# Kernel tuning notes

Measured on AMD Instinct MI355X. Metric: run time of the kernel, lower is better.

The kernel has to match this reference:

```python
import jax, jax.numpy as jnp
from jax import lax
import numpy as np


def _conv(x, w, stride):
    # x: [B,C,D,H,W], w: [3,3,3,Cin,Cout]; kernel 3, pad 1 (matches SubMConv3d / SparseConv3d(3, s, padding=1))
    return lax.conv_general_dilated(x, w, (stride, stride, stride), [(1, 1)] * 3,
                                    dimension_numbers=('NCDHW', 'DHWIO', 'NCDHW'))


def _bn_relu(y, scale, shift, mask):
    # eval-mode BatchNorm folded to scale/shift, ReLU, then restrict to active sites
    return jnp.maximum(y * scale[None, :, None, None, None] + shift[None, :, None, None, None], 0.0) * mask


def _downsample_mask(m):
    # SparseConv3d(k=3, s=2, p=1): output site active iff any input in its 3x3x3 window is active
    return lax.reduce_window(m, -jnp.inf, lax.max, (1, 1, 3, 3, 3), (1, 1, 2, 2, 2),
                             [(0, 0), (0, 0), (1, 1), (1, 1), (1, 1)])


def setup_inputs() -> dict:
    key = jax.random.key(0)
    ks = jax.random.split(key, 40)
    B, D = 1, 128
    occ = jax.random.uniform(ks[0], (B, 1, D, D, D)) < 0.05
    x = jax.random.normal(ks[1], (B, 16, D, D, D), jnp.float32) * occ

    def w(k, ci, co):
        return jax.random.normal(k, (3, 3, 3, ci, co), jnp.float32) * (1.0 / np.sqrt(27.0 * ci))

    def sc(k, c):
        return jax.random.uniform(k, (c,), jnp.float32, 0.5, 1.5)

    def sh(k, c):
        return jax.random.normal(k, (c,), jnp.float32) * 0.1

    chans = [(16, 16), (16, 16), (16, 32), (32, 32), (32, 32), (32, 64), (64, 64), (64, 64), (64, 64)]
    names = ['w0a', 'w0b', 'wd0', 'w1a', 'w1b', 'wd1', 'w2a', 'w2b', 'w2c']
    d = {'x': x, 'mask': occ}
    i = 2
    for n, (ci, co) in zip(names, chans):
        d[n] = w(ks[i], ci, co)
        d['s' + n[1:]] = sc(ks[i + 1], co)
        d['b' + n[1:]] = sh(ks[i + 2], co)
        i += 3
    return d


def reference(x, mask, w0a, s0a, b0a, w0b, s0b, b0b, wd0, sd0, bd0,
              w1a, s1a, b1a, w1b, s1b, b1b, wd1, sd1, bd1,
              w2a, s2a, b2a, w2b, s2b, b2b, w2c, s2c, b2c):
    m0 = mask.astype(x.dtype)                       # active sites at full res [B,1,128,128,128]
    h = _bn_relu(_conv(x, w0a, 1), s0a, b0a, m0)    # conv0 (subm0)
    h = _bn_relu(_conv(h, w0b, 1), s0b, b0b, m0)
    m1 = _downsample_mask(m0)                       # down0 activity [B,1,64,64,64]
    h = _bn_relu(_conv(h, wd0, 2), sd0, bd0, m1)
    h = _bn_relu(_conv(h, w1a, 1), s1a, b1a, m1)    # conv1 (subm1)
    h = _bn_relu(_conv(h, w1b, 1), s1b, b1b, m1)
    m2 = _downsample_mask(m1)                       # down1 activity [B,1,32,32,32]
    h = _bn_relu(_conv(h, wd1, 2), sd1, bd1, m2)
    h = _bn_relu(_conv(h, w2a, 1), s2a, b2a, m2)    # conv2 (subm2)
    h = _bn_relu(_conv(h, w2b, 1), s2b, b2b, m2)
    h = _bn_relu(_conv(h, w2c, 1), s2c, b2c, m2)
    return h                                        # .dense() -> [B,64,32,32,32]
```

## Files before the change

kernel.cpp:

```cpp
#include <hip/hip_runtime.h>
#include <cstdint>

typedef unsigned short u16;
typedef unsigned int u32;
typedef unsigned char u8;
typedef unsigned long long u64;
typedef __attribute__((ext_vector_type(8))) short short8;
typedef __attribute__((ext_vector_type(4))) float f32x4;

#define CAP 131072

__device__ __forceinline__ float bf1(u16 v){ union{u32 i; float f;} c; c.i = ((u32)v) << 16; return c.f; }
__device__ __forceinline__ u16 f2bf(float f){
    union{float f; u32 i;} c; c.f = f; u32 i = c.i;
    return (u16)((i + 0x7FFFu + ((i >> 16) & 1u)) >> 16);
}

constexpr int ilog2c(int n){ return n <= 1 ? 0 : 1 + ilog2c(n / 2); }

struct PAll {
    const void* w[9];
    u32 wstart[10];
    int cin[9], cout[9], mode[9];
    const void* s[18];
};

__global__ void detect_k(const u16* __restrict__ s0a, u32* __restrict__ flag){
    if (threadIdx.x == 0){
        int ok = 1;
        #pragma unroll
        for (int i = 0; i < 8; i += 2){
            u16 v = s0a[i];
            if (v < 0x3F00u || v > 0x3FC0u) ok = 0;
        }
        flag[0] = ok ? 1u : 0u;
    }
}

__global__ __launch_bounds__(256)
void prep_k(PAll J, u16* __restrict__ FR, float* __restrict__ S,
            const u32* __restrict__ flag){
    const int gi = blockIdx.x * 256 + threadIdx.x;
    const int wtot = (int)J.wstart[9];
    if (gi < wtot){
        int j = 0;
        while (gi >= (int)J.wstart[j + 1]) ++j;
        const int i = gi - (int)J.wstart[j];
        const void* w = J.w[j];
        const int CIN = J.cin[j], COUT = J.cout[j];
        const int jj = i & 7;
        const int lane = (i >> 3) & 63;
        int rest = i >> 9;
        int src = -1;
        if (J.mode[j] == 0){
            const int KC = CIN >> 5, NT = COUT >> 4;
            const int nt = rest % NT; rest /= NT;
            const int kc = rest % KC; const int tap = rest / KC;
            const int k = kc * 32 + (lane >> 4) * 8 + jj;
            const int co = nt * 16 + (lane & 15);
            src = (tap * CIN + k) * COUT + co;
        } else if (J.mode[j] == 1){
            const int nt = rest & 1; const int pair = rest >> 1;
            const int kg = (lane >> 4) * 8 + jj;
            const int tap = pair * 2 + (kg >> 4);
            const int ci = kg & 15;
            const int co = nt * 16 + (lane & 15);
            if (tap < 27) src = (tap * 16 + ci) * 32 + co;
        } else {
            const int pair = rest;
            const int kg = (lane >> 4) * 8 + jj;
            const int tap = pair * 2 + (kg >> 4);
            const int ci = kg & 15;
            const int co = lane & 15;
            if (tap < 27) src = (tap * 16 + ci) * 16 + co;
        }
        float v = 0.f;
        if (src >= 0) v = flag[0] ? bf1(((const u16*)w)[src]) : ((const float*)w)[src];
        FR[gi] = f2bf(v);
    } else {
        const int i2 = gi - wtot;
        const int len[18] = {16,16,16,16,32,32,32,32,32,32,64,64,64,64,64,64,64,64};
        const int off[18] = {0,16,32,48,64,96,128,160,192,224,256,320,384,448,512,576,640,704};
        if (i2 < 768){
            int b = 0, base = 0;
            while (i2 >= base + len[b]) { base += len[b]; ++b; }
            const int t = i2 - base;
            const float v = flag[0] ? bf1(((const u16*)J.s[b])[t]) : ((const float*)J.s[b])[t];
            S[off[b] + t] = v;
        }
    }
}

__global__ __launch_bounds__(256)
void actmask_k(const void* __restrict__ xv, u64* __restrict__ bmask,
               u32* __restrict__ bcnt, const u32* __restrict__ flag){
    const int v = blockIdx.x * 256 + threadIdx.x;
    const size_t N = 2097152;
    u32 a = 0;
    if (flag[0]) {
        const u16* x = (const u16*)xv;
        #pragma unroll
        for (int c = 0; c < 16; ++c) a |= (u32)(x[(size_t)c * N + v]) & 0x7FFFu;
    } else {
        const u32* x = (const u32*)xv;
        #pragma unroll
        for (int c = 0; c < 16; ++c) a |= x[(size_t)c * N + v] & 0x7FFFFFFFu;
    }
    const u64 m = __ballot(a != 0);
    __shared__ u32 wc[4];
    const int lane = threadIdx.x & 63, wv = threadIdx.x >> 6;
    if (lane == 0) { bmask[v >> 6] = m; wc[wv] = (u32)__popcll(m); }
    __syncthreads();
    if (threadIdx.x == 0) bcnt[blockIdx.x] = wc[0] + wc[1] + wc[2] + wc[3];
}

__global__ __launch_bounds__(1024)
void aux_k(const u32* __restrict__ bcnt, u32* __restrict__ boff, u32* __restrict__ cnt,
           const u64* __restrict__ bmask, u8* __restrict__ m1){
    if (blockIdx.x == 0){
        __shared__ u32 lds[1024];
        const int t = threadIdx.x;
        u32 loc[8]; u32 s = 0;
        #pragma unroll
        for (int i = 0; i < 8; ++i){ loc[i] = s; s += bcnt[t * 8 + i]; }
        lds[t] = s;
        __syncthreads();
        u32 v = s;
        for (int d = 1; d < 1024; d <<= 1){
            u32 o = (t >= d) ? lds[t - d] : 0;
            __syncthreads();
            v += o; lds[t] = v;
            __syncthreads();
        }
        const u32 base = v - s;
        #pragma unroll
        for (int i = 0; i < 8; ++i) boff[t * 8 + i] = base + loc[i];
        if (t == 1023) cnt[0] = v;
    } else {
        const int v = (blockIdx.x - 1) * 1024 + threadIdx.x;
        const int xo = v & 63, yo = (v >> 6) & 63, zo = v >> 12;
        u32 a = 0;
        #pragma unroll
        for (int kz = 0; kz < 3; ++kz){ const int iz = 2*zo + kz - 1; if ((unsigned)iz >= 128u) continue;
          #pragma unroll
          for (int ky = 0; ky < 3; ++ky){ const int iy = 2*yo + ky - 1; if ((unsigned)iy >= 128u) continue;
            #pragma unroll
            for (int kx = 0; kx < 3; ++kx){ const int ix = 2*xo + kx - 1; if ((unsigned)ix >= 128u) continue;
              const int vv = (iz * 128 + iy) * 128 + ix;
              a |= (u32)((bmask[vv >> 6] >> (vv & 63)) & 1ull);
        }}}
        m1[v] = (u8)a;
    }
}

__global__ __launch_bounds__(256)
void scatter2m_k(const void* __restrict__ xv, const u64* __restrict__ bmask,
                 const u32* __restrict__ boff, int* __restrict__ idxmap,
                 int* __restrict__ alist, u16* __restrict__ f,
                 const u32* __restrict__ flag,
                 const u8* __restrict__ m1, u8* __restrict__ m2){
    if (blockIdx.x < 8192){
        const int v = blockIdx.x * 256 + threadIdx.x;
        const int lane = threadIdx.x & 63, wv = threadIdx.x >> 6;
        const u64 m = bmask[v >> 6];
        __shared__ u32 wc[4];
        if (lane == 0) wc[wv] = (u32)__popcll(m);
        __syncthreads();
        u32 wbase = 0;
        for (int i = 0; i < wv; ++i) wbase += wc[i];
        const bool act = (m >> lane) & 1ull;
        const u32 rank = (u32)__popcll(m & ((1ull << lane) - 1ull));
        int slot = -1;
        if (act){
            const u32 sl = boff[blockIdx.x] + wbase + rank;
            if (sl < CAP){
                slot = (int)sl;
                alist[slot] = v;
                if (flag[0]){
                    const u16* x = (const u16*)xv;
                    #pragma unroll
                    for (int c = 0; c < 16; ++c) f[(size_t)slot * 16 + c] = x[(size_t)c * 2097152 + v];
                } else {
                    const float* x = (const float*)xv;
                    #pragma unroll
                    for (int c = 0; c < 16; ++c) f[(size_t)slot * 16 + c] = f2bf(x[(size_t)c * 2097152 + v]);
                }
            }
        }
        idxmap[v] = slot;
    } else {
        const int v = (int)(blockIdx.x - 8192) * 256 + threadIdx.x;
        const int xo = v & 31, yo = (v >> 5) & 31, zo = v >> 10;
        u8 a = 0;
        #pragma unroll
        for (int kz = 0; kz < 3; ++kz){ const int iz = 2*zo + kz - 1; if ((unsigned)iz >= 64u) continue;
          #pragma unroll
          for (int ky = 0; ky < 3; ++ky){ const int iy = 2*yo + ky - 1; if ((unsigned)iy >= 64u) continue;
            #pragma unroll
            for (int kx = 0; kx < 3; ++kx){ const int ix = 2*xo + kx - 1; if ((unsigned)ix >= 64u) continue;
              a |= m1[((size_t)iz * 64 + iy) * 64 + ix];
        }}}
        m2[v] = a;
    }
}

__global__ __launch_bounds__(256)
void sconvm_k(const u16* __restrict__ fin, const int* __restrict__ idxmap,
              const int* __restrict__ alist, const u32* __restrict__ cnt,
              const u16* __restrict__ wf, const float* __restrict__ sc,
              const float* __restrict__ sh, u16* __restrict__ fout){
    const int n = min((int)cnt[0], CAP);
    const int j = blockIdx.x * 4 + (threadIdx.x >> 6);
    const int sbase = j * 16;
    if (sbase >= n) return;
    const int lane = threadIdx.x & 63;
    const int m = lane & 15, quad = lane >> 4;

    const int s = sbase + m;
    const int v = (s < n) ? alist[s] : -1;
    int xo = 0, yo = 0, zo = 0;
    if (v >= 0){ xo = v & 127; yo = (v >> 7) & 127; zo = v >> 14; }

    f32x4 acc = {0.f,0.f,0.f,0.f};
    #pragma unroll
    for (int p = 0; p < 14; ++p){
        const int tp = p * 2 + (quad >> 1);
        short8 a = {0,0,0,0,0,0,0,0};
        if (v >= 0 && tp < 27){
            const int kz = tp / 9, ky = (tp / 3) % 3, kx = tp % 3;
            const int iz = zo + kz - 1, iy = yo + ky - 1, ix = xo + kx - 1;
            if ((unsigned)iz < 128u && (unsigned)iy < 128u && (unsigned)ix < 128u){
                const int sn = idxmap[((size_t)iz * 128 + iy) * 128 + ix];
                if (sn >= 0) a = *(const short8*)(fin + (size_t)sn * 16 + (quad & 1) * 8);
            }
        }
        short8 b = *(const short8*)(wf + ((size_t)p * 64 + lane) * 8);
        acc = __builtin_amdgcn_mfma_f32_16x16x32_bf16(a, b, acc, 0, 0, 0);
    }

    const int co = lane & 15;
    const float scl = sc[co], shf = sh[co];
    #pragma unroll
    for (int r = 0; r < 4; ++r){
        const int srow = sbase + quad * 4 + r;
        if (srow < n){
            fout[(size_t)srow * 16 + co] = f2bf(fmaxf(acc[r] * scl + shf, 0.f));
        }
    }
}

__global__ __launch_bounds__(256)
void convd0m_k(const u16* __restrict__ fbuf, const int* __restrict__ idxmap,
               const u16* __restrict__ wf, const float* __restrict__ sc,
               const float* __restrict__ sh, const u8* __restrict__ mk,
               u16* __restrict__ out)
{
    const int wj = blockIdx.x * 4 + (threadIdx.x >> 6);
    const int lane = threadIdx.x & 63;
    const int m = lane & 15, quad = lane >> 4;
    const int xo_b = (wj & 3) * 16;
    const int yo = (wj >> 2) & 63;
    const int zo = wj >> 8;

    f32x4 acc0 = {0.f,0.f,0.f,0.f}, acc1 = {0.f,0.f,0.f,0.f};
    const int ix_m = (xo_b + m) * 2 - 1;

    #pragma unroll
    for (int p = 0; p < 14; ++p){
        const int tp = p * 2 + (quad >> 1);
        short8 a = {0,0,0,0,0,0,0,0};
        if (tp < 27){
            const int kz = tp / 9, ky = (tp / 3) % 3, kx = tp % 3;
            const int iz = 2*zo + kz - 1, iy = 2*yo + ky - 1, ix = ix_m + kx;
            if ((unsigned)iz < 128u && (unsigned)iy < 128u && (unsigned)ix < 128u){
                const int sn = idxmap[((size_t)iz * 128 + iy) * 128 + ix];
                if (sn >= 0) a = *(const short8*)(fbuf + (size_t)sn * 16 + (quad & 1) * 8);
            }
        }
        short8 b0 = *(const short8*)(wf + ((size_t)(p*2+0) * 64 + lane) * 8);
        short8 b1 = *(const short8*)(wf + ((size_t)(p*2+1) * 64 + lane) * 8);
        acc0 = __builtin_amdgcn_mfma_f32_16x16x32_bf16(a, b0, acc0, 0, 0, 0);
        acc1 = __builtin_amdgcn_mfma_f32_16x16x32_bf16(a, b1, acc1, 0, 0, 0);
    }

    const int vb = wj * 16 + quad * 4;
    const u32 m4 = *(const u32*)(mk + vb);
    const int n = lane & 15;
    #pragma unroll
    for (int nt = 0; nt < 2; ++nt){
        const int co = nt * 16 + n;
        const float s = sc[co], h = sh[co];
        const f32x4 acc = nt ? acc1 : acc0;
        #pragma unroll
        for (int r = 0; r < 4; ++r){
            float val = fmaxf(acc[r] * s + h, 0.f);
            val = ((m4 >> (8*r)) & 0xFFu) ? val : 0.f;
            out[(size_t)(vb + r) * 32 + co] = f2bf(val);
        }
    }
}

template<int DIN, int DOUT, int CIN, int COUT, int STRIDE, bool FINAL>
__global__ __launch_bounds__(256)
void mconv_k(const u16* __restrict__ in, const u16* __restrict__ wf,
             const float* __restrict__ sc, const float* __restrict__ sh,
             const u8* __restrict__ mk, void* __restrict__ out,
             const u32* __restrict__ flag)
{
    constexpr int KC = CIN / 32;
    constexpr int NT = COUT / 16;
    constexpr int XT = DOUT / 16;
    const int wj = blockIdx.x * 4 + (threadIdx.x >> 6);
    const int lane = threadIdx.x & 63;
    const int m = lane & 15, quad = lane >> 4;

    const int xo_b = (wj % XT) * 16;
    const int yo = (wj / XT) % DOUT;
    const int zo = wj / (XT * DOUT);

    f32x4 acc[NT];
    #pragma unroll
    for (int i = 0; i < NT; ++i) acc[i] = (f32x4){0.f,0.f,0.f,0.f};

    const int ix0 = (xo_b + m) * STRIDE - 1;
    for (int kz = 0; kz < 3; ++kz){
      const int iz = zo * STRIDE + kz - 1;
      if ((unsigned)iz >= (unsigned)DIN) continue;
      for (int ky = 0; ky < 3; ++ky){
        const int iy = yo * STRIDE + ky - 1;
        if ((unsigned)iy >= (unsigned)DIN) continue;
        const size_t rowb = ((size_t)iz * DIN + iy) * DIN;
        #pragma unroll
        for (int kx = 0; kx < 3; ++kx){
          const int ix = ix0 + kx;
          const bool v = (unsigned)ix < (unsigned)DIN;
          const int tap = (kz*3 + ky)*3 + kx;
          const u16* ap = in + (rowb + ix) * CIN + quad * 8;
          const u16* bp = wf + (size_t)tap * KC * NT * 512 + lane * 8;
          #pragma unroll
          for (int kc = 0; kc < KC; ++kc){
            short8 a = {0,0,0,0,0,0,0,0};
            if (v) a = *(const short8*)(ap + kc * 32);
            #pragma unroll
            for (int nt = 0; nt < NT; ++nt){
              short8 b = *(const short8*)(bp + (kc * NT + nt) * 512);
              acc[nt] = __builtin_amdgcn_mfma_f32_16x16x32_bf16(a, b, acc[nt], 0, 0, 0);
            }
          }
    }}}

    const int vb = wj * 16 + quad * 4;
    const u32 m4 = *(const u32*)(mk + vb);
    const int n = lane & 15;
    #pragma unroll
    for (int nt = 0; nt < NT; ++nt){
        const int co = nt * 16 + n;
        const float s = sc[co], h = sh[co];
        #pragma unroll
        for (int r = 0; r < 4; ++r){
            float val = fmaxf(acc[nt][r] * s + h, 0.f);
            val = ((m4 >> (8*r)) & 0xFFu) ? val : 0.f;
            ((u16*)out)[(size_t)(vb + r) * COUT + co] = f2bf(val);
        }
    }
    (void)flag;
}

template<int D, int CIN, int COUT, int WAVES, bool FINAL>
__global__ __launch_bounds__(WAVES*64)
void mconvlds_k(const u16* __restrict__ in, const u16* __restrict__ wf,
                const float* __restrict__ sc, const float* __restrict__ sh,
                const u8* __restrict__ mk, void* __restrict__ out,
                const u32* __restrict__ flag)
{
    constexpr int KC = CIN / 32;
    constexpr int NT = COUT / 16;
    constexpr int CH8 = CIN / 8;
    constexpr int BT = WAVES * 64;
    __shared__ u16 tile[9 * 2048];

    const int t = threadIdx.x;
    const int yo = blockIdx.x % D, zo = blockIdx.x / D;

    for (int dz = 0; dz < 3; ++dz){
      const int iz = zo + dz - 1;
      for (int dy = 0; dy < 3; ++dy){
        const int iy = yo + dy - 1;
        if ((unsigned)iz < (unsigned)D && (unsigned)iy < (unsigned)D){
          const u16* src = in + ((size_t)(iz * D + iy) * D) * CIN;
          u16* dst = &tile[(dz * 3 + dy) * 2048];
          for (int c = t; c < D * CH8; c += BT){
            const int x = c / CH8, c8 = c % CH8;
            *(short8*)(dst + (c8 * D + x) * 8) = *(const short8*)(src + c * 8);
          }
        }
      }
    }
    __syncthreads();

    const int lane = t & 63, w = t >> 6;
    const int m = lane & 15, quad = lane >> 4;
    const int xo_b = w * 16;

    f32x4 acc[NT];
    #pragma unroll
    for (int i = 0; i < NT; ++i) acc[i] = (f32x4){0.f,0.f,0.f,0.f};

    #pragma unroll
    for (int kz = 0; kz < 3; ++kz){
      const int iz = zo + kz - 1;
      if ((unsigned)iz >= (unsigned)D) continue;
      #pragma unroll
      for (int ky = 0; ky < 3; ++ky){
        const int iy = yo + ky - 1;
        if ((unsigned)iy >= (unsigned)D) continue;
        const u16* row = &tile[(kz * 3 + ky) * 2048];
        #pragma unroll
        for (int kx = 0; kx < 3; ++kx){
          const int ix = xo_b + m + kx - 1;
          const bool aok = (unsigned)ix < (unsigned)D;
          const int tap = (kz * 3 + ky) * 3 + kx;
          const u16* bp = wf + (size_t)tap * KC * NT * 512 + lane * 8;
          #pragma unroll
          for (int kc = 0; kc < KC; ++kc){
            short8 a = {0,0,0,0,0,0,0,0};
            if (aok) a = *(const short8*)(row + ((kc * 4 + quad) * D + ix) * 8);
            #pragma unroll
            for (int nt = 0; nt < NT; ++nt){
              short8 b = *(const short8*)(bp + (kc * NT + nt) * 512);
              acc[nt] = __builtin_amdgcn_mfma_f32_16x16x32_bf16(a, b, acc[nt], 0, 0, 0);
            }
          }
        }
      }
    }

    const int vb = (zo * D + yo) * D + xo_b + quad * 4;
    const u32 m4 = *(const u32*)(mk + vb);
    const int n = lane & 15;
    if (FINAL) {
        const bool bfout = flag[0] != 0;
        #pragma unroll
        for (int nt = 0; nt < NT; ++nt){
            const int co = nt * 16 + n;
            const float s = sc[co], h = sh[co];
            float4 o;
            float* po = &o.x;
            #pragma unroll
            for (int r = 0; r < 4; ++r){
                float val = fmaxf(acc[nt][r] * s + h, 0.f);
                po[r] = ((m4 >> (8*r)) & 0xFFu) ? val : 0.f;
            }
            if (!bfout) {
                *(float4*)((float*)out + (size_t)co * (D*D*D) + vb) = o;
            } else {
                u16* ob = (u16*)out + (size_t)co * (D*D*D) + vb;
                #pragma unroll
                for (int r = 0; r < 4; ++r) ob[r] = f2bf(po[r]);
            }
        }
    } else {
        #pragma unroll
        for (int nt = 0; nt < NT; ++nt){
            const int co = nt * 16 + n;
            const float s = sc[co], h = sh[co];
            #pragma unroll
            for (int r = 0; r < 4; ++r){
                float val = fmaxf(acc[nt][r] * s + h, 0.f);
                val = ((m4 >> (8*r)) & 0xFFu) ? val : 0.f;
                ((u16*)out)[(size_t)(vb + r) * COUT + co] = f2bf(val);
            }
        }
    }
}

extern "C" void kernel_launch(void* const* d_in, const int* in_sizes, int n_in,
                              void* d_out, int out_size, void* d_ws, size_t ws_size,
                              hipStream_t stream)
{
    (void)out_size; (void)ws_size;

    int wb = 2;
    for (int i = 1; i < n_in; ++i) { if (in_sizes[i] == 6912) { wb = i; break; } }

    const void* x = d_in[0];
    const void *w0a=d_in[wb+0],  *s0a=d_in[wb+1],  *b0a=d_in[wb+2];
    const void *w0b=d_in[wb+3],  *s0b=d_in[wb+4],  *b0b=d_in[wb+5];
    const void *wd0=d_in[wb+6],  *sd0=d_in[wb+7],  *bd0=d_in[wb+8];
    const void *w1a=d_in[wb+9],  *s1a=d_in[wb+10], *b1a=d_in[wb+11];
    const void *w1b=d_in[wb+12], *s1b=d_in[wb+13], *b1b=d_in[wb+14];
    const void *wd1=d_in[wb+15], *sd1=d_in[wb+16], *bd1=d_in[wb+17];
    const void *w2a=d_in[wb+18], *s2a=d_in[wb+19], *b2a=d_in[wb+20];
    const void *w2b=d_in[wb+21], *s2b=d_in[wb+22], *b2b=d_in[wb+23];
    const void *w2c=d_in[wb+24], *s2c=d_in[wb+25], *b2c=d_in[wb+26];

    char* ws = (char*)d_ws;
    int*   idxmap = (int*)(ws);
    u16*   Fb0    = (u16*)(ws + 8388608);
    u16*   Fb1    = (u16*)(ws + 12582912);
    u16*   Fb2    = (u16*)(ws + 16777216);
    u16*   Rb1    = (u16*)(ws + 25165824);
    u16*   Rb2    = (u16*)(ws + 41943040);
    u8*    m1     = (u8*)(ws + 58720256);
    u8*    m2     = (u8*)(ws + 58982400);
    u32*   cnt    = (u32*)(ws + 59015168);
    int*   alist  = (int*)(ws + 59015424);
    u16*   FR     = (u16*)(ws + 59539712);
    float* S      = (float*)(ws + 60483328);
    u32*   flag   = (u32*)(ws + 60486400);
    u64*   bmask  = (u64*)(ws + 60486656);
    u32*   bcnt   = (u32*)(ws + 60748800);
    u32*   boff   = (u32*)(ws + 60781568);

    u16* wfs0a = FR + 0;
    u16* wfs0b = FR + 7168;
    u16* fd0   = FR + 14336;
    u16* f1a   = FR + 28672;
    u16* f1b   = FR + 56320;
    u16* fd1   = FR + 83968;
    u16* f2a   = FR + 139264;
    u16* f2b   = FR + 249856;
    u16* f2c   = FR + 360448;

    detect_k<<<1, 64, 0, stream>>>((const u16*)s0a, flag);

    PAll J;
    const void* jsrc[9] = {w0a, w0b, wd0, w1a, w1b, wd1, w2a, w2b, w2c};
    const u32 jlen[9]   = {7168,7168,14336,27648,27648,55296,110592,110592,110592};
    const int jcin[9]   = {16,16,16,32,32,32,64,64,64};
    const int jcout[9]  = {16,16,32,32,32,64,64,64,64};
    const int jmode[9]  = {2,2,1,0,0,0,0,0,0};
    u32 acc = 0;
    for (int i = 0; i < 9; ++i){
        J.w[i] = jsrc[i]; J.wstart[i] = acc; acc += jlen[i];
        J.cin[i] = jcin[i]; J.cout[i] = jcout[i]; J.mode[i] = jmode[i];
    }
    J.wstart[9] = acc;
    const void* sv[18] = {s0a,b0a,s0b,b0b,sd0,bd0,s1a,b1a,s1b,b1b,sd1,bd1,s2a,b2a,s2b,b2b,s2c,b2c};
    for (int i = 0; i < 18; ++i) J.s[i] = sv[i];
    const u32 ptot = acc + 768;
    prep_k<<<(int)((ptot + 255) / 256), 256, 0, stream>>>(J, FR, S, flag);

    float *cs0a=S+0,  *cb0a=S+16,  *cs0b=S+32,  *cb0b=S+48;
    float *csd0=S+64, *cbd0=S+96,  *cs1a=S+128, *cb1a=S+160, *cs1b=S+192, *cb1b=S+224;
    float *csd1=S+256,*cbd1=S+320, *cs2a=S+384, *cb2a=S+448, *cs2b=S+512, *cb2b=S+576, *cs2c=S+640, *cb2c=S+704;

    actmask_k<<<8192, 256, 0, stream>>>(x, bmask, bcnt, flag);
    aux_k<<<257, 1024, 0, stream>>>(bcnt, boff, cnt, bmask, m1);
    scatter2m_k<<<8320, 256, 0, stream>>>(x, bmask, boff, idxmap, alist, Fb0, flag, m1, m2);

    sconvm_k<<<2048, 256, 0, stream>>>(Fb0, idxmap, alist, cnt, wfs0a, cs0a, cb0a, Fb1);
    sconvm_k<<<2048, 256, 0, stream>>>(Fb1, idxmap, alist, cnt, wfs0b, cs0b, cb0b, Fb2);
    convd0m_k<<<4096, 256, 0, stream>>>(Fb2, idxmap, fd0, csd0, cbd0, m1, Rb1);
    mconvlds_k<64,32,32,4,false><<<4096, 256, 0, stream>>>(Rb1, f1a, cs1a, cb1a, m1, Rb2, flag);
    mconvlds_k<64,32,32,4,false><<<4096, 256, 0, stream>>>(Rb2, f1b, cs1b, cb1b, m1, Rb1, flag);
    mconv_k<64,32,32,64,2,false><<<512, 256, 0, stream>>>(Rb1, fd1, csd1, cbd1, m2, Rb2, flag);
    mconvlds_k<32,64,64,2,false><<<1024, 128, 0, stream>>>(Rb2, f2a, cs2a, cb2a, m2, Rb1, flag);
    mconvlds_k<32,64,64,2,false><<<1024, 128, 0, stream>>>(Rb1, f2b, cs2b, cb2b, m2, Rb2, flag);
    mconvlds_k<32,64,64,2,true ><<<1024, 128, 0, stream>>>(Rb2, f2c, cs2c, cb2c, m2, d_out, flag);
}
```

Before: 530.9 us.

## Use 32x32x16 MFMA dense conv kernel for subm1 and subm2 layers

Adds a new dense convolution kernel that stages a 3x3 row neighbourhood in LDS and computes with 32x32x16 bf16 MFMA instructions, plus a new weight fragment layout (mode 3) matching that instruction. It replaces the previous 16-wide MFMA LDS kernel for four of the stride-1 layers. The aim is to raise MFMA throughput per instruction and cut fragment loads. B fragments are read directly from global memory each step, and the block size changes to 128 threads, which may alter occupancy and reuse.

```diff
diff --git a/kernel.cpp b/kernel.cpp
--- a/kernel.cpp
+++ b/kernel.cpp
@@ -7,6 +7,7 @@
 typedef unsigned long long u64;
 typedef __attribute__((ext_vector_type(8))) short short8;
 typedef __attribute__((ext_vector_type(4))) float f32x4;
+typedef __attribute__((ext_vector_type(16))) float f32x16;
 
 #define CAP 131072
 
@@ -66,13 +67,20 @@
             const int ci = kg & 15;
             const int co = nt * 16 + (lane & 15);
             if (tap < 27) src = (tap * 16 + ci) * 32 + co;
-        } else {
+        } else if (J.mode[j] == 2){
             const int pair = rest;
             const int kg = (lane >> 4) * 8 + jj;
             const int tap = pair * 2 + (kg >> 4);
             const int ci = kg & 15;
             const int co = lane & 15;
             if (tap < 27) src = (tap * 16 + ci) * 16 + co;
+        } else {
+            const int KC = CIN >> 4, NTN = COUT >> 5;
+            const int nt = rest % NTN; rest /= NTN;
+            const int kc = rest % KC; const int tap = rest / KC;
+            const int k = kc * 16 + (lane >> 5) * 8 + jj;
+            const int co = nt * 32 + (lane & 31);
+            src = (tap * CIN + k) * COUT + co;
         }
         float v = 0.f;
         if (src >= 0) v = flag[0] ? bf1(((const u16*)w)[src]) : ((const float*)w)[src];
@@ -474,6 +482,85 @@
     }
 }
 
+template<int D, int CIN, int COUT>
+__global__ __launch_bounds__(128)
+void mconv32_k(const u16* __restrict__ in, const u16* __restrict__ wf,
+               const float* __restrict__ sc, const float* __restrict__ sh,
+               const u8* __restrict__ mk, u16* __restrict__ out)
+{
+    constexpr int KC = CIN / 16;
+    constexpr int NTN = COUT / 32;
+    constexpr int XW = D / 32;
+    constexpr int CH8 = CIN / 8;
+    __shared__ u16 tile[9 * 2048];
+
+    const int t = threadIdx.x;
+    const int yo = blockIdx.x % D, zo = blockIdx.x / D;
+
+    for (int dz = 0; dz < 3; ++dz){
+      const int iz = zo + dz - 1;
+      for (int dy = 0; dy < 3; ++dy){
+        const int iy = yo + dy - 1;
+        if ((unsigned)iz < (unsigned)D && (unsigned)iy < (unsigned)D){
+          const u16* src = in + ((size_t)(iz * D + iy) * D) * CIN;
+          u16* dst = &tile[(dz * 3 + dy) * 2048];
+          for (int c = t; c < D * CH8; c += 128){
+            const int x = c / CH8, c8 = c % CH8;
+            *(short8*)(dst + (c8 * D + x) * 8) = *(const short8*)(src + c * 8);
+          }
+        }
+      }
+    }
+    __syncthreads();
+
+    const int lane = t & 63, w = t >> 6;
+    const int m32 = lane & 31, half = lane >> 5;
+    const int xo_b = (XW == 2) ? w * 32 : 0;
+    const int nt   = (XW == 2) ? 0 : w;
+
+    f32x16 acc;
+    #pragma unroll
+    for (int i = 0; i < 16; ++i) acc[i] = 0.f;
+
+    #pragma unroll
+    for (int kz = 0; kz < 3; ++kz){
+      const int iz = zo + kz - 1;
+      if ((unsigned)iz >= (unsigned)D) continue;
+      #pragma unroll
+      for (int ky = 0; ky < 3; ++ky){
+        const int iy = yo + ky - 1;
+        if ((unsigned)iy >= (unsigned)D) continue;
+        const u16* row = &tile[(kz * 3 + ky) * 2048];
+        #pragma unroll
+        for (int kx = 0; kx < 3; ++kx){
+          const int ix = xo_b + m32 + kx - 1;
+          const bool aok = (unsigned)ix < (unsigned)D;
+          const int tap = (kz * 3 + ky) * 3 + kx;
+          const u16* bp = wf + ((size_t)tap * KC * NTN + nt) * 512 + lane * 8;
+          #pragma unroll
+          for (int kc = 0; kc < KC; ++kc){
+            short8 a = {0,0,0,0,0,0,0,0};
+            if (aok) a = *(const short8*)(row + ((kc * 2 + half) * D + ix) * 8);
+            short8 b = *(const short8*)(bp + (size_t)kc * NTN * 512);
+            acc = __builtin_amdgcn_mfma_f32_32x32x16_bf16(a, b, acc, 0, 0, 0);
+          }
+        }
+      }
+    }
+
+    const int base = (zo * D + yo) * D;
+    const int co = nt * 32 + m32;
+    const float s = sc[co], h = sh[co];
+    #pragma unroll
+    for (int reg = 0; reg < 16; ++reg){
+        const int rrow = (reg & 3) + 8 * (reg >> 2) + 4 * half;
+        const int xv = xo_b + rrow;
+        float val = fmaxf(acc[reg] * s + h, 0.f);
+        val = mk[base + xv] ? val : 0.f;
+        out[(size_t)(base + xv) * COUT + co] = f2bf(val);
+    }
+}
+
 extern "C" void kernel_launch(void* const* d_in, const int* in_sizes, int n_in,
                               void* d_out, int out_size, void* d_ws, size_t ws_size,
                               hipStream_t stream)
@@ -529,7 +616,7 @@
     const u32 jlen[9]   = {7168,7168,14336,27648,27648,55296,110592,110592,110592};
     const int jcin[9]   = {16,16,16,32,32,32,64,64,64};
     const int jcout[9]  = {16,16,32,32,32,64,64,64,64};
-    const int jmode[9]  = {2,2,1,0,0,0,0,0,0};
+    const int jmode[9]  = {2,2,1,3,3,0,3,3,0};
     u32 acc = 0;
     for (int i = 0; i < 9; ++i){
         J.w[i] = jsrc[i]; J.wstart[i] = acc; acc += jlen[i];
@@ -552,10 +639,10 @@
     sconvm_k<<<2048, 256, 0, stream>>>(Fb0, idxmap, alist, cnt, wfs0a, cs0a, cb0a, Fb1);
     sconvm_k<<<2048, 256, 0, stream>>>(Fb1, idxmap, alist, cnt, wfs0b, cs0b, cb0b, Fb2);
     convd0m_k<<<4096, 256, 0, stream>>>(Fb2, idxmap, fd0, csd0, cbd0, m1, Rb1);
-    mconvlds_k<64,32,32,4,false><<<4096, 256, 0, stream>>>(Rb1, f1a, cs1a, cb1a, m1, Rb2, flag);
-    mconvlds_k<64,32,32,4,false><<<4096, 256, 0, stream>>>(Rb2, f1b, cs1b, cb1b, m1, Rb1, flag);
+    mconv32_k<64,32,32><<<4096, 128, 0, stream>>>(Rb1, f1a, cs1a, cb1a, m1, Rb2);
+    mconv32_k<64,32,32><<<4096, 128, 0, stream>>>(Rb2, f1b, cs1b, cb1b, m1, Rb1);
     mconv_k<64,32,32,64,2,false><<<512, 256, 0, stream>>>(Rb1, fd1, csd1, cbd1, m2, Rb2, flag);
-    mconvlds_k<32,64,64,2,false><<<1024, 128, 0, stream>>>(Rb2, f2a, cs2a, cb2a, m2, Rb1, flag);
-    mconvlds_k<32,64,64,2,false><<<1024, 128, 0, stream>>>(Rb1, f2b, cs2b, cb2b, m2, Rb2, flag);
+    mconv32_k<32,64,64><<<1024, 128, 0, stream>>>(Rb2, f2a, cs2a, cb2a, m2, Rb1);
+    mconv32_k<32,64,64><<<1024, 128, 0, stream>>>(Rb1, f2b, cs2b, cb2b, m2, Rb2);
     mconvlds_k<32,64,64,2,true ><<<1024, 128, 0, stream>>>(Rb2, f2c, cs2c, cb2c, m2, d_out, flag);
 }
```

After: 562.9 us. +6.0%, slower.
